# Performance work log

Measured on AMD Instinct MI355X. Metric: run time of the kernel, lower is better.

Reference implementation:

```python
import jax, jax.numpy as jnp
import numpy as np

DT = 0.01        # base_dt from __init__
DT_SCALE = 1.0   # forward default


def setup_inputs() -> dict:
    key = jax.random.key(0)
    k1, k2, k3, k4, k5 = jax.random.split(key, 5)
    B, D, R = 4096, 512, 128
    x = jax.random.normal(k1, (B, D), dtype=jnp.float32)
    v = jax.random.normal(k2, (B, D), dtype=jnp.float32)
    force = jax.random.normal(k3, (B, D), dtype=jnp.float32)
    U = jax.random.normal(k4, (D, R), dtype=jnp.float32) * (1.0 / np.sqrt(D))
    W = jax.random.normal(k5, (R, D), dtype=jnp.float32) * (1.0 / np.sqrt(R))
    return {"x": x, "v": v, "force": force, "U": U, "W": W, "steps": 8}


def reference(x, v, force, U, W, steps):
    dt = DT * DT_SCALE
    # Dormand-Prince (DP5) tableau
    a21 = 1/5
    a31, a32 = 3/40, 9/40
    a41, a42, a43 = 44/45, -56/15, 32/9
    a51, a52, a53, a54 = 19372/6561, -25360/2187, 64448/6561, -212/729
    a61, a62, a63, a64, a65 = 9017/3168, -355/33, 46732/5247, 49/176, -5103/18656
    b1, b3, b4, b5, b6 = 35/384, 500/1113, 125/192, -2187/6784, 11/84

    def dynamics(tx, tv):
        # low-rank Christoffel: gamma(v, x) = ((v @ U) * (x @ U)) @ W
        acc = -jnp.einsum('br,rd->bd', (tv @ U) * (tx @ U), W)
        return acc + force

    def step(carry, _):
        cx, cv = carry
        k1x = cv
        k1v = dynamics(cx, cv)
        x2 = cx + dt * (a21 * k1x); v2 = cv + dt * (a21 * k1v)
        k2x = v2; k2v = dynamics(x2, v2)
        x3 = cx + dt * (a31 * k1x + a32 * k2x)
        v3 = cv + dt * (a31 * k1v + a32 * k2v)
        k3x = v3; k3v = dynamics(x3, v3)
        x4 = cx + dt * (a41 * k1x + a42 * k2x + a43 * k3x)
        v4 = cv + dt * (a41 * k1v + a42 * k2v + a43 * k3v)
        k4x = v4; k4v = dynamics(x4, v4)
        x5 = cx + dt * (a51 * k1x + a52 * k2x + a53 * k3x + a54 * k4x)
        v5 = cv + dt * (a51 * k1v + a52 * k2v + a53 * k3v + a54 * k4v)
        k5x = v5; k5v = dynamics(x5, v5)
        x6 = cx + dt * (a61 * k1x + a62 * k2x + a63 * k3x + a64 * k4x + a65 * k5x)
        v6 = cv + dt * (a61 * k1v + a62 * k2v + a63 * k3v + a64 * k4v + a65 * k5v)
        k6x = v6; k6v = dynamics(x6, v6)
        nx = cx + dt * (b1 * k1x + b3 * k3x + b4 * k4x + b5 * k5x + b6 * k6x)
        nv = cv + dt * (b1 * k1v + b3 * k3v + b4 * k4v + b5 * k5v + b6 * k6v)
        return (nx, nv), None

    (fx, fv), _ = jax.lax.scan(step, (x, v), None, length=steps)
    return fx, fv
```

## Files before the change

### kernel.cpp

```cpp
#include <hip/hip_runtime.h>


typedef _Float16 v8h __attribute__((ext_vector_type(8)));
typedef float v4f __attribute__((ext_vector_type(4)));
typedef unsigned short u16;
typedef unsigned int u32;

#define MFMAH __builtin_amdgcn_mfma_f32_16x16x32_f16
#define INV2048 4.8828125e-4f
#define INV256  0.00390625f

struct Tab {
  double a[7][7]; double b[7]; double A[7]; double XC[7][7]; double XF[7]; double cxc[7];
};
static constexpr Tab make_tab() {
  Tab t{};
  t.a[2][1]=1.0/5;
  t.a[3][1]=3.0/40;       t.a[3][2]=9.0/40;
  t.a[4][1]=44.0/45;      t.a[4][2]=-56.0/15;      t.a[4][3]=32.0/9;
  t.a[5][1]=19372.0/6561; t.a[5][2]=-25360.0/2187; t.a[5][3]=64448.0/6561; t.a[5][4]=-212.0/729;
  t.a[6][1]=9017.0/3168;  t.a[6][2]=-355.0/33;     t.a[6][3]=46732.0/5247; t.a[6][4]=49.0/176; t.a[6][5]=-5103.0/18656;
  t.b[1]=35.0/384; t.b[2]=0.0; t.b[3]=500.0/1113; t.b[4]=125.0/192; t.b[5]=-2187.0/6784; t.b[6]=11.0/84;
  for (int i=1;i<=6;++i){ double s=0; for(int j=1;j<i;++j) s+=t.a[i][j]; t.A[i]=s; }
  for (int i=1;i<=6;++i) for(int l=1;l<i;++l){ double s=0; for(int j=l+1;j<i;++j) s+=t.a[i][j]*t.a[j][l]; t.XC[i][l]=s; }
  for (int i=1;i<=6;++i){ double s=0; for(int j=1;j<i;++j) s+=t.a[i][j]*t.A[j]; t.XF[i]=s; }
  for (int j=1;j<=6;++j){ double s=0; for (int i=j+1;i<=6;++i) s+=t.b[i]*t.a[i][j]; t.cxc[j]=s; }
  return t;
}
static constexpr Tab TB = make_tab();

__device__ __forceinline__ int decode_steps(const void* p){
  int v = *(const int*)p;
  if (v >= 1 && v <= 512) return v;
  float f = *(const float*)p;
  if (f >= 1.f && f <= 512.f) return (int)f;
  return 8;
}
__device__ __forceinline__ void split2s(float x, _Float16& h, _Float16& l){
  h = (_Float16)x;
  l = (_Float16)((x - (float)h) * 2048.0f);
}

#define WS_GH 0
#define WS_GL 16384
#define WS_UH 32768
#define WS_UL 98304
#define WS_WH 163840
#define WS_WL 229376

__global__ __launch_bounds__(256) void k_prep1(const float* __restrict__ U,
                                               const float* __restrict__ W,
                                               _Float16* __restrict__ ws){
  const int b = blockIdx.x, tid = threadIdx.x;
  if (b < 256) {
    int idx = b*256 + tid;
    int r = idx >> 7, c = idx & 127;
    _Float16 h, l; split2s(U[idx]*256.f, h, l);
    int kb=r>>5, q=(r>>3)&3, j=r&7, nb=c>>4, cl=c&15;
    int slot = ((nb*16+kb)*64 + q*16+cl)*8 + j;
    ws[WS_UH + slot] = h; ws[WS_UL + slot] = l;
  } else {
    int idx = (b-256)*256 + tid;
    int r = idx >> 9, c = idx & 511;
    _Float16 h, l; split2s(W[idx]*256.f, h, l);
    int kb=r>>5, q=(r>>3)&3, j=r&7, nb=c>>4, cl=c&15;
    int slot = ((nb*4+kb)*64 + q*16+cl)*8 + j;
    ws[WS_WH + slot] = h; ws[WS_WL + slot] = l;
  }
}

__global__ __launch_bounds__(512) void k_prep2(const float* __restrict__ W,
                                               _Float16* __restrict__ ws){
  const int tid = threadIdx.x, b = blockIdx.x;
  const int ww = tid >> 6, lane = tid & 63, q = lane >> 4, c16 = lane & 15;
  const int nb = ww;
  const _Float16* uH = ws + WS_UH;
  const _Float16* uL = ws + WS_UL;
  v4f aH = {0,0,0,0}, aC0 = {0,0,0,0}, aC1 = {0,0,0,0};
  #pragma unroll
  for (int kb = 0; kb < 16; ++kb) {
    const float* wp = W + (b*16 + c16)*512 + kb*32 + q*8;
    float4 w0 = *(const float4*)wp;
    float4 w1 = *(const float4*)(wp + 4);
    float wv[8] = {w0.x,w0.y,w0.z,w0.w, w1.x,w1.y,w1.z,w1.w};
    v8h Ah, Al;
    #pragma unroll
    for (int j = 0; j < 8; ++j) {
      _Float16 h, l; split2s(-wv[j], h, l);
      Ah[j] = h; Al[j] = l;
    }
    int bo = ((nb*16 + kb)*64 + lane)*8;
    v8h Bh = *(const v8h*)(uH + bo);
    v8h Bl = *(const v8h*)(uL + bo);
    aH = MFMAH(Ah, Bh, aH, 0,0,0);
    if (kb & 1) {
      aC1 = MFMAH(Ah, Bl, aC1, 0,0,0);
      aC1 = MFMAH(Al, Bh, aC1, 0,0,0);
    } else {
      aC0 = MFMAH(Ah, Bl, aC0, 0,0,0);
      aC0 = MFMAH(Al, Bh, aC0, 0,0,0);
    }
  }
  #pragma unroll
  for (int r = 0; r < 4; ++r) {
    float g = aH[r] + (aC0[r] + aC1[r])*INV2048;
    _Float16 h, l; split2s(g, h, l);
    int m = b*16 + 4*q + r, n = nb*16 + c16;
    int slot = (((n>>4)*4 + (m>>5))*64 + ((m>>3)&3)*16 + (n&15))*8 + (m&7);
    ws[WS_GH + slot] = h; ws[WS_GL + slot] = l;
  }
}

#define ARENA 33280

__global__ __launch_bounds__(512,4) void dp5_main(
    const float* __restrict__ xg, const float* __restrict__ vg,
    const float* __restrict__ fg, const void* stepsp,
    const _Float16* __restrict__ ws, float* __restrict__ outg)
{
  __shared__ __align__(16) char arena[ARENA];
  _Float16* base = (_Float16*)arena;
  const _Float16* uH = ws + WS_UH;
  const _Float16* uL = ws + WS_UL;
  const _Float16* wH = ws + WS_WH;
  const _Float16* wL = ws + WS_WL;

  const int tid  = threadIdx.x;
  const int ww   = tid >> 6;
  const int lane = tid & 63;
  const int q    = lane >> 4;
  const int c16  = lane & 15;
  const int nb   = ww;
  const int kcol = nb*16 + c16;
  const int srcl = (q>>1)*16 + c16;
  const bool odd = (q & 1);
  const int rb   = blockIdx.x * 8;
  const int S    = decode_steps(stepsp);
  const float dt = 0.01f;

  v8h Gh[4], Gl[4];
  #pragma unroll
  for (int kb = 0; kb < 4; ++kb) {
    int off = ((nb*4 + kb)*64 + lane)*8;
    Gh[kb] = *(const v8h*)(ws + WS_GH + off);
    Gl[kb] = *(const v8h*)(ws + WS_GL + off);
  }

  _Float16* tH = base;
  _Float16* tL = base + 8320;
  const int r16 = tid >> 5, c0 = (tid & 31)*16;
  float xU0[2], vU0[2], fU0[2];
  for (int pass = 0; pass < 2; ++pass) {
    if (pass == 0 || r16 < 8) {
      const float* sp;
      if (pass == 0) sp = (r16 < 8) ? (xg + (rb + r16)*512) : (vg + (rb + r16 - 8)*512);
      else           sp = fg + (rb + r16)*512;
      sp += c0;
      float4 g0 = *(const float4*)(sp);
      float4 g1 = *(const float4*)(sp + 4);
      float4 g2 = *(const float4*)(sp + 8);
      float4 g3 = *(const float4*)(sp + 12);
      float vals[16] = {g0.x,g0.y,g0.z,g0.w, g1.x,g1.y,g1.z,g1.w,
                        g2.x,g2.y,g2.z,g2.w, g3.x,g3.y,g3.z,g3.w};
      v8h vh0, vh1, vl0, vl1;
      #pragma unroll
      for (int j = 0; j < 8; ++j) {
        _Float16 h, l;
        split2s(vals[j], h, l);     vh0[j] = h; vl0[j] = l;
        split2s(vals[8+j], h, l);   vh1[j] = h; vl1[j] = l;
      }
      int o = r16*520 + c0;
      *(v8h*)(tH + o) = vh0; *(v8h*)(tH + o + 8) = vh1;
      *(v8h*)(tL + o) = vl0; *(v8h*)(tL + o + 8) = vl1;
    }
    __syncthreads();
    v4f aH0={0,0,0,0}, aH1={0,0,0,0}, aC0={0,0,0,0}, aC1={0,0,0,0};
    #pragma unroll
    for (int kb = 0; kb < 16; ++kb) {
      int ao = c16*520 + kb*32 + q*8;
      v8h Ah = *(const v8h*)(tH + ao);
      v8h Al = *(const v8h*)(tL + ao);
      int bo = ((nb*16 + kb)*64 + lane)*8;
      v8h Bh = *(const v8h*)(uH + bo);
      v8h Bl = *(const v8h*)(uL + bo);
      if (kb & 1) {
        aH1 = MFMAH(Ah, Bh, aH1, 0,0,0);
        aC1 = MFMAH(Ah, Bl, aC1, 0,0,0);
        aC1 = MFMAH(Al, Bh, aC1, 0,0,0);
      } else {
        aH0 = MFMAH(Ah, Bh, aH0, 0,0,0);
        aC0 = MFMAH(Ah, Bl, aC0, 0,0,0);
        aC0 = MFMAH(Al, Bh, aC0, 0,0,0);
      }
    }
    float at0 = ((aH0[0]+aH1[0]) + (aC0[0]+aC1[0])*INV2048)*INV256;
    float at1 = ((aH0[1]+aH1[1]) + (aC0[1]+aC1[1])*INV2048)*INV256;
    float at2 = ((aH0[2]+aH1[2]) + (aC0[2]+aC1[2])*INV2048)*INV256;
    float at3 = ((aH0[3]+aH1[3]) + (aC0[3]+aC1[3])*INV2048)*INV256;
    if (pass == 0) {
      float sx0=__shfl(at0,srcl,64), sx1=__shfl(at1,srcl,64);
      float sx2=__shfl(at2,srcl,64), sx3=__shfl(at3,srcl,64);
      xU0[0] = odd ? sx2 : sx0; xU0[1] = odd ? sx3 : sx1;
      int srclv = srcl + 32;
      float sv0=__shfl(at0,srclv,64), sv1=__shfl(at1,srclv,64);
      float sv2=__shfl(at2,srclv,64), sv3=__shfl(at3,srclv,64);
      vU0[0] = odd ? sv2 : sv0; vU0[1] = odd ? sv3 : sv1;
    } else {
      float sf0=__shfl(at0,srcl,64), sf1=__shfl(at1,srcl,64);
      float sf2=__shfl(at2,srcl,64), sf3=__shfl(at3,srcl,64);
      fU0[0] = odd ? sf2 : sf0; fU0[1] = odd ? sf3 : sf1;
    }
    __syncthreads();
  }

  float cxU[2], cvU[2], kU6[6][2], Rr[2], QXa[2];
  #pragma unroll
  for (int j = 0; j < 2; ++j) {
    cxU[j] = xU0[j]; cvU[j] = vU0[j]; Rr[j] = 0.f; QXa[j] = 0.f;
    #pragma unroll
    for (int l = 0; l < 6; ++l) kU6[l][j] = 0.f;
  }

  int pb = 0;
  for (int s = 0; s < S; ++s) {
    float accX[2], accV[2], Pbs[2], Pxcs[2];
    #pragma unroll
    for (int j = 0; j < 2; ++j) { accX[j]=0.f; accV[j]=0.f; Pbs[j]=0.f; Pxcs[j]=0.f; }

    #pragma unroll
    for (int i = 1; i <= 6; ++i) {
      _Float16* bH = base + (pb ? 4352 : 0);
      _Float16* bL = bH + 2176;
      const float dtA   = dt*(float)TB.A[i];
      const float dt2XF = dt*dt*(float)TB.XF[i];
      const float bi    = (float)TB.b[i];
      const float ci    = (float)TB.cxc[i];
      #pragma unroll
      for (int j = 0; j < 2; ++j) {
        float vv = cvU[j] + dtA*fU0[j];
        float xx = cxU[j] + dtA*cvU[j] + dt2XF*fU0[j];
        #pragma unroll
        for (int l = 1; l < i; ++l) {
          vv += (dt*(float)TB.a[i][l]) * kU6[l-1][j];
          xx += (dt*dt*(float)TB.XC[i][l]) * kU6[l-1][j];
        }
        float p = vv*xx;
        Pbs[j] += bi*p; Pxcs[j] += ci*p;
        _Float16 h, l2; split2s(p, h, l2);
        int ad = (2*q + j)*136 + kcol;
        bH[ad] = h; bL[ad] = l2;
      }
      __syncthreads();
      v4f aH={0,0,0,0}, aC0={0,0,0,0}, aC1={0,0,0,0};
      #pragma unroll
      for (int kb = 0; kb < 4; ++kb) {
        int ao = c16*136 + kb*32 + q*8;
        v8h Ah = *(const v8h*)(bH + ao);
        v8h Al = *(const v8h*)(bL + ao);
        aH = MFMAH(Ah, Gh[kb], aH, 0,0,0);
        if (kb & 1) {
          aC1 = MFMAH(Ah, Gl[kb], aC1, 0,0,0);
          aC1 = MFMAH(Al, Gh[kb], aC1, 0,0,0);
        } else {
          aC0 = MFMAH(Ah, Gl[kb], aC0, 0,0,0);
          aC0 = MFMAH(Al, Gh[kb], aC0, 0,0,0);
        }
      }
      float at0 = (aH[0] + (aC0[0]+aC1[0])*INV2048)*INV256;
      float at1 = (aH[1] + (aC0[1]+aC1[1])*INV2048)*INV256;
      float at2 = (aH[2] + (aC0[2]+aC1[2])*INV2048)*INV256;
      float at3 = (aH[3] + (aC0[3]+aC1[3])*INV2048)*INV256;
      float s0v=__shfl(at0,srcl,64), s1v=__shfl(at1,srcl,64);
      float s2v=__shfl(at2,srcl,64), s3v=__shfl(at3,srcl,64);
      #pragma unroll
      for (int j = 0; j < 2; ++j) {
        float kv = j ? (odd ? s3v : s1v) : (odd ? s2v : s0v);
        kU6[i-1][j] = kv;
        accX[j] += ci*kv; accV[j] += bi*kv;
      }
      pb ^= 1;
    }

    #pragma unroll
    for (int j = 0; j < 2; ++j) {
      float nx = cxU[j] + dt*cvU[j] + dt*dt*(accX[j] + 0.5f*fU0[j]);
      cvU[j] += dt*(accV[j] + fU0[j]);
      cxU[j]  = nx;
      QXa[j] += Rr[j] + Pxcs[j];
      Rr[j]  += Pbs[j];
    }
  }

  __syncthreads();
  _Float16* RQh = base;
  _Float16* RQl = base + 2176;
  #pragma unroll
  for (int j = 0; j < 2; ++j) {
    _Float16 h, l;
    split2s(Rr[j], h, l);
    int ad = (2*q + j)*136 + kcol;
    RQh[ad] = h; RQl[ad] = l;
    split2s(QXa[j], h, l);
    int ad2 = (8 + 2*q + j)*136 + kcol;
    RQh[ad2] = h; RQl[ad2] = l;
  }
  __syncthreads();

  const float Sdt = (float)S * dt;
  #pragma unroll
  for (int cbi = 0; cbi < 4; ++cbi) {
    int cb = nb*4 + cbi;
    v4f aH={0,0,0,0}, aC0={0,0,0,0}, aC1={0,0,0,0};
    #pragma unroll
    for (int kb = 0; kb < 4; ++kb) {
      int bo = ((cb*4 + kb)*64 + lane)*8;
      v8h Bh = *(const v8h*)(wH + bo);
      v8h Bl = *(const v8h*)(wL + bo);
      int ao = c16*136 + kb*32 + q*8;
      v8h Ah = *(const v8h*)(RQh + ao);
      v8h Al = *(const v8h*)(RQl + ao);
      aH = MFMAH(Ah, Bh, aH, 0,0,0);
      if (kb & 1) {
        aC1 = MFMAH(Ah, Bl, aC1, 0,0,0);
        aC1 = MFMAH(Al, Bh, aC1, 0,0,0);
      } else {
        aC0 = MFMAH(Ah, Bl, aC0, 0,0,0);
        aC0 = MFMAH(Al, Bh, aC0, 0,0,0);
      }
    }
    float r0 = (aH[0] + (aC0[0]+aC1[0])*INV2048)*INV256;
    float r1 = (aH[1] + (aC0[1]+aC1[1])*INV2048)*INV256;
    float r2 = (aH[2] + (aC0[2]+aC1[2])*INV2048)*INV256;
    float r3 = (aH[3] + (aC0[3]+aC1[3])*INV2048)*INV256;
    float o0 = __shfl_xor(r0, 32, 64);
    float o1 = __shfl_xor(r1, 32, 64);
    float o2 = __shfl_xor(r2, 32, 64);
    float o3 = __shfl_xor(r3, 32, 64);
    if (q < 2) {
      float abv[4] = {r0, r1, r2, r3};
      float axv[4] = {o0, o1, o2, o3};
      #pragma unroll
      for (int i4 = 0; i4 < 4; ++i4) {
        int off = (rb + 4*q + i4)*512 + cb*16 + c16;
        float x0 = xg[off], v0 = vg[off], f0 = fg[off];
        outg[off]           = x0 + Sdt*v0 + 0.5f*Sdt*Sdt*f0 - dt*dt*axv[i4];
        outg[2097152 + off] = v0 + Sdt*f0 - dt*abv[i4];
      }
    }
  }
}

extern "C" void kernel_launch(void* const* d_in, const int* in_sizes, int n_in,
                              void* d_out, int out_size, void* d_ws, size_t ws_size,
                              hipStream_t stream) {
  const float* x = (const float*)d_in[0];
  const float* v = (const float*)d_in[1];
  const float* f = (const float*)d_in[2];
  const float* U = (const float*)d_in[3];
  const float* W = (const float*)d_in[4];
  _Float16* ws = (_Float16*)d_ws;

  k_prep1<<<dim3(512), dim3(256), 0, stream>>>(U, W, ws);
  k_prep2<<<dim3(8),   dim3(512), 0, stream>>>(W, ws);
  dp5_main<<<dim3(512), dim3(512), 0, stream>>>(
      x, v, f, d_in[5], ws, (float*)d_out);
}
```

Baseline: 159.6 us.

## Transpose stage GEMM so hi/lo splits share one B operand, halving MFMAs

Reorganizes the per-stage rank-space GEMM so the products p are stored as hi/lo rows of a single fp16 tile used as the B operand, with the G matrix hi/lo parts as A. This cuts the per-stage MFMA count from 12 to 8 and the LDS reads from two tiles to one. Each active lane now owns 4 rank values instead of 2, so the state is transposed through LDS once before the step loop. Only half the lanes (c16<8) do the elementwise stage work, and the lo contribution is recombined with a shfl_xor. The risk is divergence and lower lane utilization in the elementwise part, plus possible accuracy changes from the new hi/lo combination.

```diff
diff --git a/kernel.cpp b/kernel.cpp
--- a/kernel.cpp
+++ b/kernel.cpp
@@ -2,6 +2,7 @@
 
 
 typedef _Float16 v8h __attribute__((ext_vector_type(8)));
+typedef _Float16 v4h __attribute__((ext_vector_type(4)));
 typedef float v4f __attribute__((ext_vector_type(4)));
 typedef unsigned short u16;
 typedef unsigned int u32;
@@ -213,96 +214,112 @@
     __syncthreads();
   }
 
-  float cxU[2], cvU[2], kU6[6][2], Rr[2], QXa[2];
-  #pragma unroll
-  for (int j = 0; j < 2; ++j) {
-    cxU[j] = xU0[j]; cvU[j] = vU0[j]; Rr[j] = 0.f; QXa[j] = 0.f;
+  float cxU4[4], cvU4[4], fU4[4];
+  {
+    float* T = (float*)arena;
+    #pragma unroll
+    for (int p2 = 0; p2 < 3; ++p2) {
+      float i0 = (p2==0) ? xU0[0] : (p2==1) ? vU0[0] : fU0[0];
+      float i1 = (p2==0) ? xU0[1] : (p2==1) ? vU0[1] : fU0[1];
+      T[(2*q + 0)*132 + kcol] = i0;
+      T[(2*q + 1)*132 + kcol] = i1;
+      __syncthreads();
+      if (c16 < 8) {
+        float4 t4 = *(const float4*)(T + c16*132 + nb*16 + 4*q);
+        float* o = (p2==0) ? cxU4 : (p2==1) ? cvU4 : fU4;
+        o[0]=t4.x; o[1]=t4.y; o[2]=t4.z; o[3]=t4.w;
+      }
+      __syncthreads();
+    }
+  }
+
+  float kU6[6][4], Rr4[4], QXa4[4];
+  #pragma unroll
+  for (int j = 0; j < 4; ++j) {
+    Rr4[j] = 0.f; QXa4[j] = 0.f;
     #pragma unroll
     for (int l = 0; l < 6; ++l) kU6[l][j] = 0.f;
   }
 
   int pb = 0;
   for (int s = 0; s < S; ++s) {
-    float accX[2], accV[2], Pbs[2], Pxcs[2];
-    #pragma unroll
-    for (int j = 0; j < 2; ++j) { accX[j]=0.f; accV[j]=0.f; Pbs[j]=0.f; Pxcs[j]=0.f; }
+    float accX[4], accV[4], Pbs[4], Pxcs[4];
+    #pragma unroll
+    for (int j = 0; j < 4; ++j) { accX[j]=0.f; accV[j]=0.f; Pbs[j]=0.f; Pxcs[j]=0.f; }
 
     #pragma unroll
     for (int i = 1; i <= 6; ++i) {
-      _Float16* bH = base + (pb ? 4352 : 0);
-      _Float16* bL = bH + 2176;
+      _Float16* bT = base + (pb ? 2176 : 0);
       const float dtA   = dt*(float)TB.A[i];
       const float dt2XF = dt*dt*(float)TB.XF[i];
       const float bi    = (float)TB.b[i];
       const float ci    = (float)TB.cxc[i];
-      #pragma unroll
-      for (int j = 0; j < 2; ++j) {
-        float vv = cvU[j] + dtA*fU0[j];
-        float xx = cxU[j] + dtA*cvU[j] + dt2XF*fU0[j];
+      if (c16 < 8) {
+        v4h hh, ll;
         #pragma unroll
-        for (int l = 1; l < i; ++l) {
-          vv += (dt*(float)TB.a[i][l]) * kU6[l-1][j];
-          xx += (dt*dt*(float)TB.XC[i][l]) * kU6[l-1][j];
+        for (int j2 = 0; j2 < 4; ++j2) {
+          float vv = cvU4[j2] + dtA*fU4[j2];
+          float xx = cxU4[j2] + dtA*cvU4[j2] + dt2XF*fU4[j2];
+          #pragma unroll
+          for (int l = 1; l < i; ++l) {
+            vv += (dt*(float)TB.a[i][l]) * kU6[l-1][j2];
+            xx += (dt*dt*(float)TB.XC[i][l]) * kU6[l-1][j2];
+          }
+          float p = vv*xx;
+          Pbs[j2] += bi*p; Pxcs[j2] += ci*p;
+          _Float16 h, l2; split2s(p, h, l2);
+          hh[j2] = h; ll[j2] = l2;
         }
-        float p = vv*xx;
-        Pbs[j] += bi*p; Pxcs[j] += ci*p;
-        _Float16 h, l2; split2s(p, h, l2);
-        int ad = (2*q + j)*136 + kcol;
-        bH[ad] = h; bL[ad] = l2;
+        *(v4h*)(bT + c16*136 + nb*16 + 4*q)     = hh;
+        *(v4h*)(bT + (8+c16)*136 + nb*16 + 4*q) = ll;
       }
       __syncthreads();
-      v4f aH={0,0,0,0}, aC0={0,0,0,0}, aC1={0,0,0,0};
+      v4f C1 = {0,0,0,0}, C2 = {0,0,0,0};
       #pragma unroll
       for (int kb = 0; kb < 4; ++kb) {
-        int ao = c16*136 + kb*32 + q*8;
-        v8h Ah = *(const v8h*)(bH + ao);
-        v8h Al = *(const v8h*)(bL + ao);
-        aH = MFMAH(Ah, Gh[kb], aH, 0,0,0);
-        if (kb & 1) {
-          aC1 = MFMAH(Ah, Gl[kb], aC1, 0,0,0);
-          aC1 = MFMAH(Al, Gh[kb], aC1, 0,0,0);
-        } else {
-          aC0 = MFMAH(Ah, Gl[kb], aC0, 0,0,0);
-          aC0 = MFMAH(Al, Gh[kb], aC0, 0,0,0);
-        }
-      }
-      float at0 = (aH[0] + (aC0[0]+aC1[0])*INV2048)*INV256;
-      float at1 = (aH[1] + (aC0[1]+aC1[1])*INV2048)*INV256;
-      float at2 = (aH[2] + (aC0[2]+aC1[2])*INV2048)*INV256;
-      float at3 = (aH[3] + (aC0[3]+aC1[3])*INV2048)*INV256;
-      float s0v=__shfl(at0,srcl,64), s1v=__shfl(at1,srcl,64);
-      float s2v=__shfl(at2,srcl,64), s3v=__shfl(at3,srcl,64);
+        v8h B = *(const v8h*)(bT + c16*136 + kb*32 + q*8);
+        C1 = MFMAH(Gh[kb], B, C1, 0,0,0);
+        C2 = MFMAH(Gl[kb], B, C2, 0,0,0);
+      }
       #pragma unroll
-      for (int j = 0; j < 2; ++j) {
-        float kv = j ? (odd ? s3v : s1v) : (odd ? s2v : s0v);
-        kU6[i-1][j] = kv;
-        accX[j] += ci*kv; accV[j] += bi*kv;
+      for (int r = 0; r < 4; ++r) {
+        float lo = __shfl_xor(C1[r], 8, 64);
+        float kv = (C1[r] + (lo + C2[r])*INV2048)*INV256;
+        kU6[i-1][r] = kv;
+        accX[r] += ci*kv; accV[r] += bi*kv;
       }
       pb ^= 1;
     }
 
     #pragma unroll
-    for (int j = 0; j < 2; ++j) {
-      float nx = cxU[j] + dt*cvU[j] + dt*dt*(accX[j] + 0.5f*fU0[j]);
-      cvU[j] += dt*(accV[j] + fU0[j]);
-      cxU[j]  = nx;
-      QXa[j] += Rr[j] + Pxcs[j];
-      Rr[j]  += Pbs[j];
+    for (int j = 0; j < 4; ++j) {
+      float nx = cxU4[j] + dt*cvU4[j] + dt*dt*(accX[j] + 0.5f*fU4[j]);
+      cvU4[j] += dt*(accV[j] + fU4[j]);
+      cxU4[j]  = nx;
+      QXa4[j] += Rr4[j] + Pxcs[j];
+      Rr4[j]  += Pbs[j];
     }
   }
 
   __syncthreads();
   _Float16* RQh = base;
   _Float16* RQl = base + 2176;
-  #pragma unroll
-  for (int j = 0; j < 2; ++j) {
-    _Float16 h, l;
-    split2s(Rr[j], h, l);
-    int ad = (2*q + j)*136 + kcol;
-    RQh[ad] = h; RQl[ad] = l;
-    split2s(QXa[j], h, l);
-    int ad2 = (8 + 2*q + j)*136 + kcol;
-    RQh[ad2] = h; RQl[ad2] = l;
+  if (c16 < 8) {
+    v4h h4, l4;
+    #pragma unroll
+    for (int j2 = 0; j2 < 4; ++j2) {
+      _Float16 h, l; split2s(Rr4[j2], h, l);
+      h4[j2] = h; l4[j2] = l;
+    }
+    *(v4h*)(RQh + c16*136 + nb*16 + 4*q) = h4;
+    *(v4h*)(RQl + c16*136 + nb*16 + 4*q) = l4;
+    #pragma unroll
+    for (int j2 = 0; j2 < 4; ++j2) {
+      _Float16 h, l; split2s(QXa4[j2], h, l);
+      h4[j2] = h; l4[j2] = l;
+    }
+    *(v4h*)(RQh + (8+c16)*136 + nb*16 + 4*q) = h4;
+    *(v4h*)(RQl + (8+c16)*136 + nb*16 + 4*q) = l4;
   }
   __syncthreads();
 
```

Result: slower. 168.1 us (+5.3%).
